# Kernel tuning notes

Hardware: AMD Instinct MI355X
Metric: run time of the kernel (lower is better)

## Reference

```python
import jax, jax.numpy as jnp
import numpy as np

B = 4096
D = 1024
NUM_CLASSES = 100
TEMPERATURE = 0.5
EPS = 1e-12  # matches F.normalize default eps


def setup_inputs() -> dict:
    key = jax.random.key(0)
    k1, k2, k3 = jax.random.split(key, 3)
    emb_i = jax.random.normal(k1, (B, D), dtype=jnp.float32)
    emb_j = jax.random.normal(k2, (B, D), dtype=jnp.float32)
    labels = jax.random.randint(k3, (B,), 0, NUM_CLASSES, dtype=jnp.int32)
    return {"emb_i": emb_i, "emb_j": emb_j, "labels": labels}


def _l2_normalize(x):
    # F.normalize(x, dim=1): x / max(||x||, eps)
    n = jnp.sqrt(jnp.sum(x * x, axis=1, keepdims=True))
    return x / jnp.maximum(n, EPS)


def reference(emb_i, emb_j, labels):
    z_i = _l2_normalize(emb_i)
    z_j = _l2_normalize(emb_j)
    reps = jnp.concatenate([z_i, z_j], axis=0)          # [2B, D]
    # cosine similarity of already-unit vectors == dot product (GEMM instead
    # of the O(N^2 D) broadcasted elementwise form in the torch code)
    sim = jnp.einsum("nd,md->nm", reps, reps)           # [2B, 2B]

    n2 = 2 * B
    neg_mask = 1.0 - jnp.eye(n2, dtype=sim.dtype)       # exclude self-pairs
    label_t = jnp.concatenate([labels, labels], axis=0)  # [2B]
    ws = (label_t[:, None] == label_t[None, :]).astype(sim.dtype) * neg_mask

    e = jnp.exp(sim / TEMPERATURE)                      # [2B, 2B]
    nominator = jnp.sum(ws * e, axis=1)                 # [2B]
    denominator = jnp.sum(neg_mask * e, axis=1)         # [2B]
    loss_partial = -jnp.log(nominator / denominator)
    return jnp.sum(loss_partial) / (2 * B)
```

## Files before the change

### kernel.cpp

```cpp
#include <hip/hip_runtime.h>
#include <hip/hip_bf16.h>
#include <hip/hip_fp8.h>


#define BHALF 4096
#define N2 8192
#define DK 1024
#define DKB 512
#define TILE 128
#define BKB 64
#define NTILE 64
#define NBLK 2080

typedef __attribute__((ext_vector_type(16))) float f32x16;
typedef __attribute__((ext_vector_type(4))) int v4i;
typedef __attribute__((ext_vector_type(8))) int v8i;
typedef unsigned char u8;
typedef unsigned short u16;

#define EXP_SCALE4 0.0028177637517362566f
#define UNIT_SCALE 0x7f7f7f7f

#define WAITVM(n) asm volatile("s_waitcnt vmcnt(" #n ")" ::: "memory")
#define BAR()     asm volatile("s_barrier" ::: "memory")

static __device__ __forceinline__ unsigned nib4(float x) {
    unsigned s = (__builtin_bit_cast(unsigned, x) >> 31) << 3;
    float a = fminf(fabsf(x), 6.0f);
    unsigned c;
    if (a < 2.0f)      c = (unsigned)lrintf(a * 2.0f);
    else if (a < 4.0f) c = (unsigned)lrintf(a) + 2u;
    else               c = (a < 5.0f) ? 6u : 7u;
    return s | c;
}

__global__ __launch_bounds__(256) void normalize_kernel(
    const float* __restrict__ emb_i, const float* __restrict__ emb_j,
    u16* __restrict__ reps, float* __restrict__ nomden,
    float* __restrict__ out) {
    int idx = blockIdx.x * 256 + threadIdx.x;
    if (idx < 2 * N2) nomden[idx] = 0.0f;
    if (idx == 0) out[0] = 0.0f;
    int r = blockIdx.x * 4 + (threadIdx.x >> 6);
    int lane = threadIdx.x & 63;
    const float* src = (r < BHALF) ? (emb_i + (size_t)r * DK)
                                   : (emb_j + (size_t)(r - BHALF) * DK);
    const float4* srcv = (const float4*)src;
    float4 v[4];
    float s = 0.f;
#pragma unroll
    for (int k = 0; k < 4; ++k) {
        v[k] = srcv[k * 64 + lane];
        s += v[k].x * v[k].x + v[k].y * v[k].y +
             v[k].z * v[k].z + v[k].w * v[k].w;
    }
#pragma unroll
    for (int m = 1; m <= 32; m <<= 1) s += __shfl_xor(s, m, 64);
    float scale = 32.0f / fmaxf(sqrtf(s), 1e-12f);
    u16* dst = reps + (size_t)r * 256;
#pragma unroll
    for (int k = 0; k < 4; ++k) {
        unsigned p = nib4(v[k].x * scale) |
                     (nib4(v[k].y * scale) << 4) |
                     (nib4(v[k].z * scale) << 8) |
                     (nib4(v[k].w * scale) << 12);
        dst[k * 64 + lane] = (u16)p;
    }
}

__global__ __launch_bounds__(256, 4) void gemm_loss_kernel(
    const u8* __restrict__ reps, const int* __restrict__ labels,
    float* __restrict__ nom, float* __restrict__ den) {
    __shared__ __align__(16) u8 A_s[2][TILE * BKB];
    __shared__ __align__(16) u8 B_s[2][TILE * BKB];

    int g = blockIdx.x;
    int rem = (g & 7) * 260 + (g >> 3);
    int bi = 0;
    while (rem >= NTILE - bi) { rem -= NTILE - bi; ++bi; }
    int bj = bi + rem;
    int rowBase = bi * TILE;
    int colBase = bj * TILE;

    int tid = threadIdx.x;
    int w = tid >> 6;
    int lane = tid & 63;
    int wm = w >> 1, wn = w & 1;
    int hk = lane >> 5;
    int l31 = lane & 31;

    f32x16 acc[2][2];
#pragma unroll
    for (int i = 0; i < 2; ++i)
#pragma unroll
        for (int j = 0; j < 2; ++j)
#pragma unroll
            for (int r = 0; r < 16; ++r) acc[i][j][r] = 0.0f;

    int srow = lane >> 2;
    int sbg = (lane & 3) ^ ((srow ^ (srow >> 2)) & 3);
    const u8* gA = reps + (size_t)(rowBase + w * 32 + srow) * DKB + sbg * 16;
    const u8* gB = reps + (size_t)(colBase + w * 32 + srow) * DKB + sbg * 16;

    int rswz = (l31 ^ (l31 >> 2)) & 3;
    unsigned aOff[2][2], bOff[2][2];
#pragma unroll
    for (int i = 0; i < 2; ++i) {
#pragma unroll
        for (int ks = 0; ks < 2; ++ks) {
            int ra = (wm * 64 + i * 32 + l31) * BKB;
            aOff[i][ks] = ra + (((ks * 2 + hk) ^ rswz) << 4);
            int rb = (wn * 64 + i * 32 + l31) * BKB;
            bOff[i][ks] = rb + (((ks * 2 + hk) ^ rswz) << 4);
        }
    }

#define STAGE(buf, kt)                                                       \
    {                                                                        \
        _Pragma("unroll")                                                    \
        for (int c = 0; c < 2; ++c) {                                        \
            int chunk = 2 * w + c;                                           \
            __builtin_amdgcn_global_load_lds(                                \
                (const __attribute__((address_space(1))) void*)              \
                    (gA + (size_t)c * 16 * DKB + (kt) * BKB),                \
                (__attribute__((address_space(3))) void*)                    \
                    &A_s[buf][chunk * 1024], 16, 0, 0);                      \
            __builtin_amdgcn_global_load_lds(                                \
                (const __attribute__((address_space(1))) void*)              \
                    (gB + (size_t)c * 16 * DKB + (kt) * BKB),                \
                (__attribute__((address_space(3))) void*)                    \
                    &B_s[buf][chunk * 1024], 16, 0, 0);                      \
        }                                                                    \
    }
#define COMPUTE(buf)                                                         \
    {                                                                        \
        _Pragma("unroll")                                                    \
        for (int ks = 0; ks < 2; ++ks) {                                     \
            v8i aF[2], bF[2];                                                \
            _Pragma("unroll")                                                \
            for (int i = 0; i < 2; ++i) {                                    \
                v4i a4 = *(const v4i*)&A_s[buf][aOff[i][ks]];                \
                aF[i] = __builtin_shufflevector(a4, a4, 0,1,2,3,0,1,2,3);    \
                v4i b4 = *(const v4i*)&B_s[buf][bOff[i][ks]];                \
                bF[i] = __builtin_shufflevector(b4, b4, 0,1,2,3,0,1,2,3);    \
            }                                                                \
            _Pragma("unroll")                                                \
            for (int i = 0; i < 2; ++i)                                      \
                _Pragma("unroll")                                            \
                for (int j = 0; j < 2; ++j)                                  \
                    acc[i][j] =                                              \
                        __builtin_amdgcn_mfma_scale_f32_32x32x64_f8f6f4(     \
                            aF[i], bF[j], acc[i][j], 4, 4,                   \
                            0, UNIT_SCALE, 0, UNIT_SCALE);                   \
        }                                                                    \
    }

    STAGE(0, 0)
    STAGE(1, 1)
    for (int kt = 0; kt < 4; kt += 2) {
        WAITVM(4); BAR();
        COMPUTE(0)
        BAR();
        STAGE(0, kt + 2)
        WAITVM(4); BAR();
        COMPUTE(1)
        BAR();
        STAGE(1, kt + 3)
    }
    WAITVM(4); BAR();
    COMPUTE(0)
    BAR();
    STAGE(0, 6)
    WAITVM(4); BAR();
    COMPUTE(1)
    BAR();
    STAGE(1, 7)
    WAITVM(4); BAR();
    COMPUTE(0)
    WAITVM(0); BAR();
    COMPUTE(1)
#undef STAGE
#undef COMPUTE

    bool offd = (bi != bj);
    int lc[2], gcol[2];
#pragma unroll
    for (int j = 0; j < 2; ++j) {
        gcol[j] = colBase + wn * 64 + j * 32 + l31;
        lc[j] = labels[gcol[j] & (BHALF - 1)];
    }
    float vD[32], vN[32];
    float colD[2] = {0.f, 0.f}, colN[2] = {0.f, 0.f};
#pragma unroll
    for (int i = 0; i < 2; ++i) {
#pragma unroll
        for (int reg = 0; reg < 16; ++reg) {
            int rowIn = (reg & 3) + 8 * (reg >> 2) + 4 * hk;
            int grow = rowBase + wm * 64 + i * 32 + rowIn;
            int labr = labels[grow & (BHALF - 1)];
            float rD = 0.f, rN = 0.f;
#pragma unroll
            for (int j = 0; j < 2; ++j) {
                float e = exp2f(acc[i][j][reg] * EXP_SCALE4);
                if (grow == gcol[j]) e = 0.f;
                bool m = (lc[j] == labr);
                rD += e; if (m) rN += e;
                colD[j] += e; if (m) colN[j] += e;
            }
            vD[i * 16 + reg] = rD;
            vN[i * 16 + reg] = rN;
        }
    }
#pragma unroll
    for (int step = 0; step < 5; ++step) {
        const int m = 16 >> step;
        const int h = 16 >> step;
        bool up = (l31 & m) != 0;
#pragma unroll
        for (int k = 0; k < h; ++k) {
            float sD = up ? vD[k] : vD[k + h];
            float sN = up ? vN[k] : vN[k + h];
            float kD = up ? vD[k + h] : vD[k];
            float kN = up ? vN[k + h] : vN[k];
            vD[k] = kD + __shfl_xor(sD, m, 64);
            vN[k] = kN + __shfl_xor(sN, m, 64);
        }
    }
    {
        int grow = rowBase + wm * 64 + (l31 >> 4) * 32 +
                   ((l31 & 3) + 8 * ((l31 >> 2) & 3) + 4 * hk);
        atomicAdd(&den[grow], vD[0]);
        atomicAdd(&nom[grow], vN[0]);
    }
    if (offd) {
#pragma unroll
        for (int j = 0; j < 2; ++j) {
            float cd = colD[j] + __shfl_xor(colD[j], 32, 64);
            float cn = colN[j] + __shfl_xor(colN[j], 32, 64);
            if (hk == 0) {
                atomicAdd(&den[gcol[j]], cd);
                atomicAdd(&nom[gcol[j]], cn);
            }
        }
    }
}

__global__ __launch_bounds__(256) void finalize_kernel(
    const float* __restrict__ nom, const float* __restrict__ den,
    float* __restrict__ out) {
    int idx = blockIdx.x * 256 + threadIdx.x;
    int t = threadIdx.x;
    float s = 0.f;
    if (idx < N2) s = logf(den[idx]) - logf(nom[idx]);
#pragma unroll
    for (int m = 1; m <= 32; m <<= 1) s += __shfl_xor(s, m, 64);
    __shared__ float red[4];
    if ((t & 63) == 0) red[t >> 6] = s;
    __syncthreads();
    if (t == 0)
        atomicAdd(out, (red[0] + red[1] + red[2] + red[3]) / (float)N2);
}

extern "C" void kernel_launch(void* const* d_in, const int* in_sizes, int n_in,
                              void* d_out, int out_size, void* d_ws, size_t ws_size,
                              hipStream_t stream) {
    const float* emb_i = (const float*)d_in[0];
    const float* emb_j = (const float*)d_in[1];
    const int* labels  = (const int*)d_in[2];
    float* out = (float*)d_out;

    char* ws = (char*)d_ws;
    u8* reps   = (u8*)ws;
    float* nom = (float*)(ws + (size_t)N2 * DKB);
    float* den = nom + N2;

    normalize_kernel<<<2048, 256, 0, stream>>>(emb_i, emb_j, (u16*)reps,
                                               nom, out);
    gemm_loss_kernel<<<NBLK, 256, 0, stream>>>(reps, labels, nom, den);
    finalize_kernel<<<(N2 + 255) / 256, 256, 0, stream>>>(nom, den, out);
}
```

Measured before the change: 120.7 us.

## Replace global float atomics with per-tile partial sums reduced in finalize

```diff
diff --git a/kernel.cpp b/kernel.cpp
--- a/kernel.cpp
+++ b/kernel.cpp
@@ -36,10 +36,8 @@
 
 __global__ __launch_bounds__(256) void normalize_kernel(
     const float* __restrict__ emb_i, const float* __restrict__ emb_j,
-    u16* __restrict__ reps, float* __restrict__ nomden,
-    float* __restrict__ out) {
+    u16* __restrict__ reps, float* __restrict__ out) {
     int idx = blockIdx.x * 256 + threadIdx.x;
-    if (idx < 2 * N2) nomden[idx] = 0.0f;
     if (idx == 0) out[0] = 0.0f;
     int r = blockIdx.x * 4 + (threadIdx.x >> 6);
     int lane = threadIdx.x & 63;
@@ -70,9 +68,10 @@
 
 __global__ __launch_bounds__(256, 4) void gemm_loss_kernel(
     const u8* __restrict__ reps, const int* __restrict__ labels,
-    float* __restrict__ nom, float* __restrict__ den) {
+    float* __restrict__ parts) {
     __shared__ __align__(16) u8 A_s[2][TILE * BKB];
     __shared__ __align__(16) u8 B_s[2][TILE * BKB];
+    __shared__ float red[2][2][128];
 
     int g = blockIdx.x;
     int rem = (g & 7) * 260 + (g >> 3);
@@ -226,11 +225,14 @@
             vN[k] = kN + __shfl_xor(sN, m, 64);
         }
     }
+    ((float*)red)[tid] = 0.0f;
+    ((float*)red)[tid + 256] = 0.0f;
+    __syncthreads();
     {
-        int grow = rowBase + wm * 64 + (l31 >> 4) * 32 +
-                   ((l31 & 3) + 8 * ((l31 >> 2) & 3) + 4 * hk);
-        atomicAdd(&den[grow], vD[0]);
-        atomicAdd(&nom[grow], vN[0]);
+        int rowOff = wm * 64 + (l31 >> 4) * 32 +
+                     ((l31 & 3) + 8 * ((l31 >> 2) & 3) + 4 * hk);
+        atomicAdd(&red[0][0][rowOff], vN[0]);
+        atomicAdd(&red[1][0][rowOff], vD[0]);
     }
     if (offd) {
 #pragma unroll
@@ -238,24 +240,38 @@
             float cd = colD[j] + __shfl_xor(colD[j], 32, 64);
             float cn = colN[j] + __shfl_xor(colN[j], 32, 64);
             if (hk == 0) {
-                atomicAdd(&den[gcol[j]], cd);
-                atomicAdd(&nom[gcol[j]], cn);
+                int colOff = wn * 64 + j * 32 + l31;
+                atomicAdd(&red[0][1][colOff], cn);
+                atomicAdd(&red[1][1][colOff], cd);
             }
         }
     }
+    __syncthreads();
+    if (tid < 128) {
+        parts[((size_t)bj * 2 + 0) * N2 + rowBase + tid] = red[0][0][tid];
+        parts[((size_t)bj * 2 + 1) * N2 + rowBase + tid] = red[1][0][tid];
+    } else if (offd) {
+        int t2 = tid - 128;
+        parts[((size_t)bi * 2 + 0) * N2 + colBase + t2] = red[0][1][t2];
+        parts[((size_t)bi * 2 + 1) * N2 + colBase + t2] = red[1][1][t2];
+    }
 }
 
 __global__ __launch_bounds__(256) void finalize_kernel(
-    const float* __restrict__ nom, const float* __restrict__ den,
-    float* __restrict__ out) {
-    int idx = blockIdx.x * 256 + threadIdx.x;
+    const float* __restrict__ parts, float* __restrict__ out) {
+    int row = blockIdx.x * 256 + threadIdx.x;
     int t = threadIdx.x;
-    float s = 0.f;
-    if (idx < N2) s = logf(den[idx]) - logf(nom[idx]);
-#pragma unroll
-    for (int m = 1; m <= 32; m <<= 1) s += __shfl_xor(s, m, 64);
+    float n = 0.f, d = 0.f;
+#pragma unroll 8
+    for (int s = 0; s < NTILE; ++s) {
+        n += parts[((size_t)s * 2 + 0) * N2 + row];
+        d += parts[((size_t)s * 2 + 1) * N2 + row];
+    }
+    float sv = logf(d) - logf(n);
+#pragma unroll
+    for (int m = 1; m <= 32; m <<= 1) sv += __shfl_xor(sv, m, 64);
     __shared__ float red[4];
-    if ((t & 63) == 0) red[t >> 6] = s;
+    if ((t & 63) == 0) red[t >> 6] = sv;
     __syncthreads();
     if (t == 0)
         atomicAdd(out, (red[0] + red[1] + red[2] + red[3]) / (float)N2);
@@ -270,12 +286,10 @@
     float* out = (float*)d_out;
 
     char* ws = (char*)d_ws;
-    u8* reps   = (u8*)ws;
-    float* nom = (float*)(ws + (size_t)N2 * DKB);
-    float* den = nom + N2;
-
-    normalize_kernel<<<2048, 256, 0, stream>>>(emb_i, emb_j, (u16*)reps,
-                                               nom, out);
-    gemm_loss_kernel<<<NBLK, 256, 0, stream>>>(reps, labels, nom, den);
-    finalize_kernel<<<(N2 + 255) / 256, 256, 0, stream>>>(nom, den, out);
-}
+    u8* reps    = (u8*)ws;
+    float* parts = (float*)(ws + (size_t)N2 * DKB);
+
+    normalize_kernel<<<2048, 256, 0, stream>>>(emb_i, emb_j, (u16*)reps, out);
+    gemm_loss_kernel<<<NBLK, 256, 0, stream>>>(reps, labels, parts);
+    finalize_kernel<<<(N2 + 255) / 256, 256, 0, stream>>>(parts, out);
+}
```

Result: slower. 133.0 us (+10.2%).
